# Performance work log

Measured on AMD Instinct MI355X. Metric: run time of the kernel, lower is better.

The kernel has to match this reference:

```python
import jax, jax.numpy as jnp
import numpy as np

B, H, W, K, A = 4096, 32, 32, 20, 4


def setup_inputs() -> dict:
    key = jax.random.key(0)
    k_wall, k_agent, k_goal, k_phi, k_l1, k_l2 = jax.random.split(key, 6)
    # obs channels: 0 = wall/feature map (random), 1 = one-hot agent pos, 2 = one-hot goal pos
    walls = jax.random.uniform(k_wall, (B, H, W), dtype=jnp.float32)
    agent_idx = jax.random.randint(k_agent, (B,), 0, H * W)
    goal_idx = jax.random.randint(k_goal, (B,), 0, H * W)
    agent = jax.nn.one_hot(agent_idx, H * W, dtype=jnp.float32).reshape(B, H, W)
    goal = jax.nn.one_hot(goal_idx, H * W, dtype=jnp.float32).reshape(B, H, W)
    obs = jnp.stack([walls, agent, goal], axis=-1)  # (B,H,W,3)
    obs_flat = obs.reshape(B, H * W * 3)
    din = H * W * 3
    return {
        "obs_flat": obs_flat,
        "Phi_w": jax.random.normal(k_phi, (din, 2 * H * W), dtype=jnp.float32) * 0.02,
        "Phi_b": jnp.zeros((2 * H * W,), jnp.float32),
        "L1_w": jax.random.normal(k_l1, (36, 16), dtype=jnp.float32) * 0.1,
        "L1_b": jnp.zeros((16,), jnp.float32),
        "L2_w": jax.random.normal(k_l2, (16, A), dtype=jnp.float32) * 0.1,
        "L2_b": jnp.zeros((A,), jnp.float32),
    }


def _mvprop(r, p):
    # K-step value propagation: V <- max(V, r + p*(best 4-neighbor V - r))
    # p = sigmoid(...) >= 0, so max over the 4 shifted nv values equals nv of the max shift.
    def body(V, _):
        pv = jnp.pad(V, ((0, 0), (1, 1), (1, 1)))
        nbr = jnp.maximum(
            jnp.maximum(pv[:, :-2, 1:-1], pv[:, 2:, 1:-1]),   # up, down
            jnp.maximum(pv[:, 1:-1, :-2], pv[:, 1:-1, 2:]),   # left, right
        )
        return jnp.maximum(V, r + p * (nbr - r)), None
    V, _ = jax.lax.scan(body, r, None, length=K)
    return V


def reference(obs_flat, Phi_w, Phi_b, L1_w, L1_b, L2_w, L2_b):
    b = obs_flat.shape[0]
    obs = obs_flat.reshape(b, H, W, 3)
    phi = jax.nn.sigmoid(obs_flat @ Phi_w + Phi_b).reshape(b, H, W, 2)
    r, p = phi[..., 0], phi[..., 1]
    V = _mvprop(r, p)  # (b,H,W)
    obs_val = jnp.concatenate([obs, V[..., None]], axis=-1)  # (b,H,W,4)
    padded = jnp.pad(obs_val, ((0, 0), (1, 1), (1, 1), (0, 0)))
    # agent position: exactly one nonzero in channel 1 per sample -> argmax
    idx = jnp.argmax(obs[..., 1].reshape(b, -1), axis=1)
    pi, pj = idx // W, idx % W
    # 3x3 neighborhood around agent in padded grid (start = pos+1-1 = pos)
    def slice_one(ov, i, j):
        return jax.lax.dynamic_slice(ov, (i, j, 0), (3, 3, 4))
    sel = jax.vmap(slice_one)(padded, pi, pj)  # (b,3,3,4)
    h = jax.nn.relu(sel.reshape(b, 36) @ L1_w + L1_b)
    logit = h @ L2_w + L2_b
    return logit
```

## Files before the change

kernel.cpp:

```cpp
#include <hip/hip_runtime.h>
#include <hip/hip_fp16.h>

#define BATCH 4096
#define HH 32
#define WW 32
#define KPROP 20
#define NACT 4
#define DIN 3072
#define DPHI 2048
#define HWC 1024
#define KC 1024
#define TILE_ELEMS (16 * KC)

typedef _Float16 h8_t __attribute__((ext_vector_type(8)));
typedef _Float16 h4_t __attribute__((ext_vector_type(4)));
typedef float f32x4 __attribute__((ext_vector_type(4)));

__device__ inline float sigmoidf(float x) { return 1.0f / (1.0f + __expf(-x)); }

__device__ inline float dpp_shr1(float x) {
    return __int_as_float(__builtin_amdgcn_update_dpp(
        0, __float_as_int(x), 0x111, 0xF, 0xF, true));
}
__device__ inline float dpp_shl1(float x) {
    return __int_as_float(__builtin_amdgcn_update_dpp(
        0, __float_as_int(x), 0x101, 0xF, 0xF, true));
}

__device__ inline size_t pack_off(int row, int k) {
    return (size_t)(row >> 4) * TILE_ELEMS + (k >> 3) * 128 + (row & 15) * 8 + (k & 7);
}

__global__ __launch_bounds__(256) void prep_fused_kernel(
    const float* __restrict__ obs,
    const float* __restrict__ Phi_w,
    _Float16* __restrict__ A_pack,
    _Float16* __restrict__ B_pack,
    _Float16* __restrict__ Pag,
    int* __restrict__ aidx, int* __restrict__ gidx)
{
    if (blockIdx.x < BATCH) {
        const int t = blockIdx.x * 256 + threadIdx.x;
        const int b = t >> 8;
        const int c0 = (t & 255) * 4;
        const float* src = obs + (size_t)b * DIN + 3 * c0;
        const float4 f0 = *(const float4*)(src);
        const float4 f1 = *(const float4*)(src + 4);
        const float4 f2 = *(const float4*)(src + 8);
        h4_t w;
        w[0] = (_Float16)f0.x; w[1] = (_Float16)f0.w;
        w[2] = (_Float16)f1.z; w[3] = (_Float16)f2.y;
        *(h4_t*)(A_pack + pack_off(b, c0)) = w;
        if (f0.y > 0.5f) aidx[b] = c0;
        if (f1.x > 0.5f) aidx[b] = c0 + 1;
        if (f1.w > 0.5f) aidx[b] = c0 + 2;
        if (f2.z > 0.5f) aidx[b] = c0 + 3;
        if (f0.z > 0.5f) gidx[b] = c0;
        if (f1.y > 0.5f) gidx[b] = c0 + 1;
        if (f2.x > 0.5f) gidx[b] = c0 + 2;
        if (f2.w > 0.5f) gidx[b] = c0 + 3;
    } else {
        const int bid = blockIdx.x - BATCH;
        const int ni = bid & 63;
        const int ci = bid >> 6;
        const int tx = threadIdx.x & 31;
        const int ty = threadIdx.x >> 5;
        #pragma unroll
        for (int s = 0; s < 4; s++) {
            const int r = ty + 8 * s;
            const int c = ci * 32 + r;
            const int n = ni * 32 + tx;
            const float w0 = Phi_w[(size_t)(3 * c) * DPHI + n];
            Pag[(size_t)c * DPHI + n]         = (_Float16)Phi_w[(size_t)(3 * c + 1) * DPHI + n];
            Pag[(size_t)(HWC + c) * DPHI + n] = (_Float16)Phi_w[(size_t)(3 * c + 2) * DPHI + n];
            B_pack[pack_off(n, c)] = (_Float16)w0;
        }
    }
}

__global__ __launch_bounds__(256) void gemm_pre_kernel(
    const _Float16* __restrict__ A_pack,
    const _Float16* __restrict__ B_pack,
    const float* __restrict__ bias,
    _Float16* __restrict__ pre)
{
    const int tid  = threadIdx.x;
    const int lane = tid & 63;
    const int wid  = tid >> 6;
    const int cb = blockIdx.x & 7;
    const int rb = blockIdx.x >> 3;
    const int m0 = rb * 64;
    const int n0 = cb * 256 + wid * 64;
    const int lm = lane & 15;
    const int kq = lane >> 4;

    const _Float16* Abase = A_pack + (size_t)(rb * 4) * TILE_ELEMS + 8 * lane;
    const _Float16* Bbase = B_pack + (size_t)(cb * 16 + wid * 4) * TILE_ELEMS + 8 * lane;

    f32x4 acc[4][4] = {};
    h8_t a0[4], b0[4], a1[4], b1[4], a2[4], b2[4], a3[4], b3[4];

    #pragma unroll
    for (int i = 0; i < 4; i++) {
        a0[i] = *(const h8_t*)(Abase + i * TILE_ELEMS);
        b0[i] = *(const h8_t*)(Bbase + i * TILE_ELEMS);
        a1[i] = *(const h8_t*)(Abase + i * TILE_ELEMS + 32 * 16);
        b1[i] = *(const h8_t*)(Bbase + i * TILE_ELEMS + 32 * 16);
        a2[i] = *(const h8_t*)(Abase + i * TILE_ELEMS + 64 * 16);
        b2[i] = *(const h8_t*)(Bbase + i * TILE_ELEMS + 64 * 16);
        a3[i] = *(const h8_t*)(Abase + i * TILE_ELEMS + 96 * 16);
        b3[i] = *(const h8_t*)(Bbase + i * TILE_ELEMS + 96 * 16);
    }

    #define COMPUTE(AB, BB)                                               \
        _Pragma("unroll")                                                 \
        for (int mt = 0; mt < 4; mt++)                                    \
            _Pragma("unroll")                                             \
            for (int nt = 0; nt < 4; nt++)                                \
                acc[mt][nt] = __builtin_amdgcn_mfma_f32_16x16x32_f16(     \
                    AB[mt], BB[nt], acc[mt][nt], 0, 0, 0);

    #define PREFETCH(AB, BB, KOFF)                                        \
        if ((KOFF) < KC) {                                                \
            _Pragma("unroll")                                             \
            for (int i = 0; i < 4; i++) {                                 \
                AB[i] = *(const h8_t*)(Abase + i * TILE_ELEMS + (KOFF) * 16); \
                BB[i] = *(const h8_t*)(Bbase + i * TILE_ELEMS + (KOFF) * 16); \
            }                                                             \
        }

    for (int k0 = 0; k0 < KC; k0 += 128) {
        COMPUTE(a0, b0); PREFETCH(a0, b0, k0 + 128);
        COMPUTE(a1, b1); PREFETCH(a1, b1, k0 + 160);
        COMPUTE(a2, b2); PREFETCH(a2, b2, k0 + 192);
        COMPUTE(a3, b3); PREFETCH(a3, b3, k0 + 224);
    }
    #undef COMPUTE
    #undef PREFETCH

    #pragma unroll
    for (int nt = 0; nt < 4; nt++) {
        const int col = n0 + nt * 16 + lm;
        const float bcol = bias[col];
        #pragma unroll
        for (int mt = 0; mt < 4; mt++) {
            #pragma unroll
            for (int r = 0; r < 4; r++) {
                const int row = m0 + mt * 16 + kq * 4 + r;
                pre[(size_t)row * DPHI + col] = (_Float16)(acc[mt][nt][r] + bcol);
            }
        }
    }
}

__global__ __launch_bounds__(256, 4) void vprop_head_kernel(
    const _Float16* __restrict__ pre,
    const _Float16* __restrict__ Pag,
    const float* __restrict__ obs,
    const int* __restrict__ aidx,
    const int* __restrict__ gidx,
    const float* __restrict__ L1w,
    const float* __restrict__ L1b,
    const float* __restrict__ L2w,
    const float* __restrict__ L2b,
    float* __restrict__ out)
{
    __shared__ __align__(16) float Vg[4][HWC];
    __shared__ float sel[4][36], hbuf[4][16];

    const int tid  = threadIdx.x;
    const int w    = tid >> 6;
    const int lane = tid & 63;
    const int b    = blockIdx.x * 4 + w;
    const int bi   = lane & 15;
    const int bj   = lane >> 4;
    const int ai = aidx[b];
    const int gi = gidx[b];

    const _Float16* pb = pre + (size_t)b * DPHI;
    const _Float16* ra = Pag + (size_t)ai * DPHI;
    const _Float16* rg = Pag + (size_t)(HWC + gi) * DPHI;

    float v[2][8], p[2][8], a[2][8];
    #pragma unroll
    for (int r = 0; r < 2; r++) {
        const int off = 64 * (2 * bi + r) + 16 * bj;
        const h8_t ph0 = *(const h8_t*)(pb + off), ph1 = *(const h8_t*)(pb + off + 8);
        const h8_t pa0 = *(const h8_t*)(ra + off), pa1 = *(const h8_t*)(ra + off + 8);
        const h8_t pg0 = *(const h8_t*)(rg + off), pg1 = *(const h8_t*)(rg + off + 8);
        #pragma unroll
        for (int c = 0; c < 4; c++) {
            const float rv = sigmoidf((float)ph0[2*c]   + (float)pa0[2*c]   + (float)pg0[2*c]);
            const float pv = sigmoidf((float)ph0[2*c+1] + (float)pa0[2*c+1] + (float)pg0[2*c+1]);
            v[r][c] = rv; p[r][c] = pv; a[r][c] = rv * (1.0f - pv);
            const float rv2 = sigmoidf((float)ph1[2*c]   + (float)pa1[2*c]   + (float)pg1[2*c]);
            const float pv2 = sigmoidf((float)ph1[2*c+1] + (float)pa1[2*c+1] + (float)pg1[2*c+1]);
            v[r][c+4] = rv2; p[r][c+4] = pv2; a[r][c+4] = rv2 * (1.0f - pv2);
        }
    }

    for (int it = 0; it < KPROP; it++) {
        float uh[8], dh[8], lh[2], rh[2];
        #pragma unroll
        for (int c = 0; c < 8; c++) {
            uh[c] = dpp_shr1(v[1][c]);
            dh[c] = dpp_shl1(v[0][c]);
        }
        #pragma unroll
        for (int r = 0; r < 2; r++) {
            lh[r] = __shfl(v[r][7], lane - 16);
            rh[r] = __shfl(v[r][0], lane + 16);
            if (bj == 0) lh[r] = 0.0f;
            if (bj == 3) rh[r] = 0.0f;
        }
        float nb[2][8];
        #pragma unroll
        for (int c = 0; c < 8; c++) {
            const float lf0 = (c == 0) ? lh[0] : v[0][c-1];
            const float rt0 = (c == 7) ? rh[0] : v[0][c+1];
            const float lf1 = (c == 0) ? lh[1] : v[1][c-1];
            const float rt1 = (c == 7) ? rh[1] : v[1][c+1];
            nb[0][c] = fmaxf(fmaxf(uh[c], v[1][c]), fmaxf(lf0, rt0));
            nb[1][c] = fmaxf(fmaxf(v[0][c], dh[c]), fmaxf(lf1, rt1));
        }
        #pragma unroll
        for (int r = 0; r < 2; r++)
            #pragma unroll
            for (int c = 0; c < 8; c++)
                v[r][c] = fmaxf(v[r][c], fmaf(p[r][c], nb[r][c], a[r][c]));
    }

    #pragma unroll
    for (int r = 0; r < 2; r++) {
        float4 lo, hi;
        lo.x = v[r][0]; lo.y = v[r][1]; lo.z = v[r][2]; lo.w = v[r][3];
        hi.x = v[r][4]; hi.y = v[r][5]; hi.z = v[r][6]; hi.w = v[r][7];
        const int base = (2 * bi + r) * 32 + 8 * bj;
        *(float4*)&Vg[w][base]     = lo;
        *(float4*)&Vg[w][base + 4] = hi;
    }
    __syncthreads();

    const int pi = ai >> 5, pj = ai & 31;
    if (lane < 36) {
        const int cell = lane >> 2;
        const int ch = lane & 3;
        const int di = pi + cell / 3 - 1;
        const int dj = pj + cell % 3 - 1;
        float vv = 0.0f;
        if (di >= 0 && di < HH && dj >= 0 && dj < WW) {
            const int c = di * WW + dj;
            vv = (ch < 3) ? obs[(size_t)b * DIN + 3 * c + ch] : Vg[w][c];
        }
        sel[w][lane] = vv;
    }
    __syncthreads();

    if (lane < 16) {
        float h = L1b[lane];
        #pragma unroll
        for (int k = 0; k < 36; k++) h += sel[w][k] * L1w[k * 16 + lane];
        hbuf[w][lane] = fmaxf(h, 0.0f);
    }
    __syncthreads();

    if (lane < 4) {
        float o = L2b[lane];
        #pragma unroll
        for (int t = 0; t < 16; t++) o += hbuf[w][t] * L2w[t * 4 + lane];
        out[(size_t)b * NACT + lane] = o;
    }
}

extern "C" void kernel_launch(void* const* d_in, const int* in_sizes, int n_in,
                              void* d_out, int out_size, void* d_ws, size_t ws_size,
                              hipStream_t stream) {
    const float* obs   = (const float*)d_in[0];
    const float* Phi_w = (const float*)d_in[1];
    const float* Phi_b = (const float*)d_in[2];
    const float* L1w   = (const float*)d_in[3];
    const float* L1b   = (const float*)d_in[4];
    const float* L2w   = (const float*)d_in[5];
    const float* L2b   = (const float*)d_in[6];
    float* out = (float*)d_out;

    char* ws = (char*)d_ws;
    _Float16* pre    = (_Float16*)ws;
    _Float16* A_pack = (_Float16*)(ws + 16777216);
    _Float16* B_pack = (_Float16*)(ws + 25165824);
    _Float16* Pag    = (_Float16*)(ws + 29360128);
    int* aidx = (int*)(ws + 37748736);
    int* gidx = aidx + BATCH;

    prep_fused_kernel<<<BATCH + 2048, 256, 0, stream>>>(obs, Phi_w, A_pack, B_pack, Pag, aidx, gidx);
    gemm_pre_kernel<<<512, 256, 0, stream>>>(A_pack, B_pack, Phi_b, pre);
    vprop_head_kernel<<<BATCH / 4, 256, 0, stream>>>(pre, Pag, obs, aidx, gidx,
                                                     L1w, L1b, L2w, L2b, out);
}
```

Before: 201.3 us.

## Stage shared A panel in LDS via direct global-to-LDS loads in GEMM

The GEMM kernel now copies the block's A panel into shared memory in two K-halves using global_load_lds, so all four waves read A fragments from LDS instead of each fetching them from global memory. B fragments remain register double-buffered from global memory, with a shallower prefetch depth than before. The grid becomes a 2D dim3(8,64), with the same block-to-tile mapping. This reduces redundant global A traffic, at the cost of 64KB of LDS per block, which limits occupancy, and extra barriers between halves.

```diff
diff --git a/kernel.cpp b/kernel.cpp
--- a/kernel.cpp
+++ b/kernel.cpp
@@ -84,59 +84,73 @@
     const float* __restrict__ bias,
     _Float16* __restrict__ pre)
 {
+    __shared__ _Float16 As[4 * 8192];
+
     const int tid  = threadIdx.x;
     const int lane = tid & 63;
     const int wid  = tid >> 6;
-    const int cb = blockIdx.x & 7;
-    const int rb = blockIdx.x >> 3;
-    const int m0 = rb * 64;
-    const int n0 = cb * 256 + wid * 64;
+    const int m0 = blockIdx.y * 64;
+    const int n0 = blockIdx.x * 256 + wid * 64;
     const int lm = lane & 15;
     const int kq = lane >> 4;
 
-    const _Float16* Abase = A_pack + (size_t)(rb * 4) * TILE_ELEMS + 8 * lane;
-    const _Float16* Bbase = B_pack + (size_t)(cb * 16 + wid * 4) * TILE_ELEMS + 8 * lane;
+    const _Float16* Apanel = A_pack + (size_t)(blockIdx.y * 4) * TILE_ELEMS;
+    const _Float16* Bbase  = B_pack + (size_t)(blockIdx.x * 16 + wid * 4) * TILE_ELEMS + 8 * lane;
 
     f32x4 acc[4][4] = {};
-    h8_t a0[4], b0[4], a1[4], b1[4], a2[4], b2[4], a3[4], b3[4];
+    h8_t a0[4], a1[4], b0[4], b1[4];
+
+    #define STAGE(H)                                                          \
+        _Pragma("unroll")                                                     \
+        for (int mt = 0; mt < 4; mt++)                                        \
+            _Pragma("unroll")                                                 \
+            for (int c = 0; c < 4; c++)                                       \
+                __builtin_amdgcn_global_load_lds(                             \
+                    (const __attribute__((address_space(1))) void*)           \
+                        (Apanel + mt * TILE_ELEMS + (H) * 8192 + c * 2048 + tid * 8), \
+                    (__attribute__((address_space(3))) void*)                 \
+                        (As + mt * 8192 + c * 2048 + tid * 8), 16, 0, 0);
+
+    #define AFRAG(AB, KL)                                                     \
+        _Pragma("unroll")                                                     \
+        for (int i = 0; i < 4; i++)                                           \
+            AB[i] = *(const h8_t*)(As + i * 8192 + (KL) * 16 + 8 * lane);
+
+    #define BFRAG(BB, KG)                                                     \
+        _Pragma("unroll")                                                     \
+        for (int i = 0; i < 4; i++)                                           \
+            BB[i] = *(const h8_t*)(Bbase + i * TILE_ELEMS + (KG) * 16);
+
+    #define COMPUTE(AB, BB)                                                   \
+        _Pragma("unroll")                                                     \
+        for (int mt = 0; mt < 4; mt++)                                        \
+            _Pragma("unroll")                                                 \
+            for (int nt = 0; nt < 4; nt++)                                    \
+                acc[mt][nt] = __builtin_amdgcn_mfma_f32_16x16x32_f16(         \
+                    AB[mt], BB[nt], acc[mt][nt], 0, 0, 0);
+
+    STAGE(0);
+    BFRAG(b0, 0); BFRAG(b1, 32);
+    __syncthreads();
 
     #pragma unroll
-    for (int i = 0; i < 4; i++) {
-        a0[i] = *(const h8_t*)(Abase + i * TILE_ELEMS);
-        b0[i] = *(const h8_t*)(Bbase + i * TILE_ELEMS);
-        a1[i] = *(const h8_t*)(Abase + i * TILE_ELEMS + 32 * 16);
-        b1[i] = *(const h8_t*)(Bbase + i * TILE_ELEMS + 32 * 16);
-        a2[i] = *(const h8_t*)(Abase + i * TILE_ELEMS + 64 * 16);
-        b2[i] = *(const h8_t*)(Bbase + i * TILE_ELEMS + 64 * 16);
-        a3[i] = *(const h8_t*)(Abase + i * TILE_ELEMS + 96 * 16);
-        b3[i] = *(const h8_t*)(Bbase + i * TILE_ELEMS + 96 * 16);
-    }
-
-    #define COMPUTE(AB, BB)                                               \
-        _Pragma("unroll")                                                 \
-        for (int mt = 0; mt < 4; mt++)                                    \
-            _Pragma("unroll")                                             \
-            for (int nt = 0; nt < 4; nt++)                                \
-                acc[mt][nt] = __builtin_amdgcn_mfma_f32_16x16x32_f16(     \
-                    AB[mt], BB[nt], acc[mt][nt], 0, 0, 0);
-
-    #define PREFETCH(AB, BB, KOFF)                                        \
-        if ((KOFF) < KC) {                                                \
-            _Pragma("unroll")                                             \
-            for (int i = 0; i < 4; i++) {                                 \
-                AB[i] = *(const h8_t*)(Abase + i * TILE_ELEMS + (KOFF) * 16); \
-                BB[i] = *(const h8_t*)(Bbase + i * TILE_ELEMS + (KOFF) * 16); \
-            }                                                             \
-        }
-
-    for (int k0 = 0; k0 < KC; k0 += 128) {
-        COMPUTE(a0, b0); PREFETCH(a0, b0, k0 + 128);
-        COMPUTE(a1, b1); PREFETCH(a1, b1, k0 + 160);
-        COMPUTE(a2, b2); PREFETCH(a2, b2, k0 + 192);
-        COMPUTE(a3, b3); PREFETCH(a3, b3, k0 + 224);
-    }
+    for (int h = 0; h < 2; h++) {
+        if (h) { __syncthreads(); STAGE(1); __syncthreads(); }
+        AFRAG(a0, 0); AFRAG(a1, 32);
+        for (int kl = 0; kl < 512; kl += 64) {
+            const int kg = h * 512 + kl;
+            COMPUTE(a0, b0);
+            if (kl + 64 < 512) { AFRAG(a0, kl + 64); }
+            if (kg + 64 < KC)  { BFRAG(b0, kg + 64); }
+            COMPUTE(a1, b1);
+            if (kl + 96 < 512) { AFRAG(a1, kl + 96); }
+            if (kg + 96 < KC)  { BFRAG(b1, kg + 96); }
+        }
+    }
+    #undef STAGE
+    #undef AFRAG
+    #undef BFRAG
     #undef COMPUTE
-    #undef PREFETCH
 
     #pragma unroll
     for (int nt = 0; nt < 4; nt++) {
@@ -293,7 +307,7 @@
     int* gidx = aidx + BATCH;
 
     prep_fused_kernel<<<BATCH + 2048, 256, 0, stream>>>(obs, Phi_w, A_pack, B_pack, Pag, aidx, gidx);
-    gemm_pre_kernel<<<512, 256, 0, stream>>>(A_pack, B_pack, Phi_b, pre);
+    gemm_pre_kernel<<<dim3(8, 64), 256, 0, stream>>>(A_pack, B_pack, Phi_b, pre);
     vprop_head_kernel<<<BATCH / 4, 256, 0, stream>>>(pre, Pag, obs, aidx, gidx,
                                                      L1w, L1b, L2w, L2b, out);
 }
```

Measured after the change: 166.6 us. -17.3%, faster.
